# Kernel tuning notes

Hardware: AMD Instinct MI355X
Metric: run time of the kernel (lower is better)

Reference implementation:

```python
import math
import jax, jax.numpy as jnp
import numpy as np

NUM_HEADS = 16
BASE = 10000.0


def _rope_sin_cos(seq_len, head_dim):
    # theta_j = pos / base^(2j/dim), j in [0, dim//2)
    j = jnp.arange(head_dim // 2, dtype=jnp.float32)
    inv_freq = jnp.power(jnp.float32(BASE), -2.0 * j / head_dim)  # [d/2]
    pos = jnp.arange(seq_len, dtype=jnp.float32)
    ang = pos[:, None] * inv_freq[None, :]          # [S, d/2]
    sin, cos = jnp.sin(ang), jnp.cos(ang)
    # interleave-repeat each entry twice: [S, d]
    sin2 = jnp.stack([sin, sin], axis=-1).reshape(seq_len, head_dim)
    cos2 = jnp.stack([cos, cos], axis=-1).reshape(seq_len, head_dim)
    return sin2, cos2


def _apply_rope(x, sin2, cos2):
    # x: [B, H, S, d]; rotate-half interleaved: (-x1, x0, -x3, x2, ...)
    x_even, x_odd = x[..., 0::2], x[..., 1::2]
    rot = jnp.stack([-x_odd, x_even], axis=-1).reshape(x.shape)
    return x * cos2 + rot * sin2


def setup_inputs() -> dict:
    key = jax.random.key(0)
    ks = jax.random.split(key, 9)
    B, S, H = 2, 2048, 2048
    sc = 1.0 / math.sqrt(H)
    return {
        "hidden_state": jax.random.normal(ks[0], (B, S, H), jnp.float32),
        "Wq": jax.random.normal(ks[1], (H, H), jnp.float32) * sc,
        "bq": jax.random.normal(ks[2], (H,), jnp.float32) * 0.01,
        "Wk": jax.random.normal(ks[3], (H, H), jnp.float32) * sc,
        "bk": jax.random.normal(ks[4], (H,), jnp.float32) * 0.01,
        "Wv": jax.random.normal(ks[5], (H, H), jnp.float32) * sc,
        "bv": jax.random.normal(ks[6], (H,), jnp.float32) * 0.01,
        "Wo": jax.random.normal(ks[7], (H, H), jnp.float32) * sc,
        "bo": jax.random.normal(ks[8], (H,), jnp.float32) * 0.01,
    }


def reference(hidden_state, Wq, bq, Wk, bk, Wv, bv, Wo, bo):
    B, S, H = hidden_state.shape
    nh = NUM_HEADS
    hd = H // nh

    def proj(W, b):
        y = jnp.einsum('bsh,hd->bsd', hidden_state, W) + b
        return y.reshape(B, S, nh, hd).transpose(0, 2, 1, 3)  # [B,nh,S,hd]

    q = proj(Wq, bq)
    k = proj(Wk, bk)
    v = proj(Wv, bv)

    sin2, cos2 = _rope_sin_cos(S, hd)  # [S, hd]
    q = _apply_rope(q, sin2, cos2)
    k = _apply_rope(k, sin2, cos2)

    scale = 1.0 / math.sqrt(hd)
    attn = jnp.einsum('bhqd,bhkd->bhqk', q, k) * scale  # [B,nh,S,S]
    attn = jax.nn.softmax(attn, axis=-1)
    out = jnp.einsum('bhqk,bhkd->bhqd', attn, v)
    out = out.transpose(0, 2, 1, 3).reshape(B, S, H)
    return jnp.einsum('bsh,hd->bsd', out, Wo) + bo
```

## Files before the change

### kernel.cpp

```cpp
#include <hip/hip_runtime.h>
#include <math.h>


typedef __bf16 bf16;
typedef __attribute__((ext_vector_type(8))) __bf16 bf16x8;
typedef __attribute__((ext_vector_type(4))) __bf16 bf16x4;
typedef __attribute__((ext_vector_type(4))) float f32x4;

#define S_LEN 2048
#define NHEAD 16
#define HD 128

__device__ __forceinline__ f32x4 mfma16(bf16x8 a, bf16x8 b, f32x4 c) {
    return __builtin_amdgcn_mfma_f32_16x16x32_bf16(a, b, c, 0, 0, 0);
}

__global__ __launch_bounds__(256) void transpose_cvt(const float* __restrict__ W,
                                                     bf16* __restrict__ Wt,
                                                     int Kd, int Nd) {
    __shared__ float tile[32][33];
    const int tx = threadIdx.x & 31, ty = threadIdx.x >> 5;
    const int bn = blockIdx.x * 32, bk = blockIdx.y * 32;
#pragma unroll
    for (int r = 0; r < 32; r += 8)
        tile[ty + r][tx] = W[(size_t)(bk + ty + r) * Nd + bn + tx];
    __syncthreads();
#pragma unroll
    for (int r = 0; r < 32; r += 8)
        Wt[(size_t)(bn + ty + r) * Kd + bk + tx] = (bf16)tile[tx][ty + r];
}

__global__ __launch_bounds__(256)
void prep(const float* __restrict__ Wq, const float* __restrict__ Wk,
          const float* __restrict__ Wv, const float* __restrict__ Wo,
          bf16* __restrict__ Wt3, bf16* __restrict__ WoT,
          const float* __restrict__ hs, bf16* __restrict__ Xb,
          float* __restrict__ stab, float* __restrict__ ctab) {
    const int z = blockIdx.z;
    const int id = blockIdx.y * 64 + blockIdx.x;
    const int t = threadIdx.x;
    if (z == 4) {
        const int g = id * 256 + t;
        if (g < 262144) {
            const int s = g >> 7, d = g & 127;
            const float invf = exp2f(-0.20762050593046013f * (float)(d >> 1));
            float sn, cs;
            sincosf((float)s * invf, &sn, &cs);
            stab[g] = sn;
            ctab[g] = cs;
        }
        return;
    }
    if (z == 5) {
        const size_t i = ((size_t)id * 256 + t) * 8;
        const float4 v0 = *(const float4*)(hs + i);
        const float4 v1 = *(const float4*)(hs + i + 4);
        bf16x8 o;
        o[0] = (bf16)v0.x; o[1] = (bf16)v0.y; o[2] = (bf16)v0.z; o[3] = (bf16)v0.w;
        o[4] = (bf16)v1.x; o[5] = (bf16)v1.y; o[6] = (bf16)v1.z; o[7] = (bf16)v1.w;
        *(bf16x8*)(Xb + i) = o;
        return;
    }
    __shared__ float tile[32][33];
    const float* W = (z == 0) ? Wq : (z == 1) ? Wk : (z == 2) ? Wv : Wo;
    bf16* Wt = (z < 3) ? (Wt3 + (size_t)z * 2048 * 2048) : WoT;
    const int tx = t & 31, ty = t >> 5;
    const int bn = blockIdx.x * 32, bk = blockIdx.y * 32;
#pragma unroll
    for (int r = 0; r < 32; r += 8)
        tile[ty + r][tx] = W[(size_t)(bk + ty + r) * 2048 + bn + tx];
    __syncthreads();
#pragma unroll
    for (int r = 0; r < 32; r += 8)
        Wt[(size_t)(bn + ty + r) * 2048 + bk + tx] = (bf16)tile[tx][ty + r];
}

__global__ __launch_bounds__(256, 3)
void gemm_qkv(const bf16* __restrict__ A, const bf16* __restrict__ Bt,
              const float* __restrict__ bq, const float* __restrict__ bk,
              const float* __restrict__ bv, bf16* __restrict__ Qo,
              bf16* __restrict__ Ko, bf16* __restrict__ Vo,
              const float* __restrict__ stab, const float* __restrict__ ctab) {
    const int K = 2048;
    __shared__ __align__(16) bf16 smem[17408];
    bf16* As = smem;
    bf16* Bs = smem + 8192;
    const int t = threadIdx.x;
    const int w = t >> 6, l = t & 63;
    const int lr = l & 15, lq = l >> 4;
    const int m0 = blockIdx.y * 128, n0 = blockIdx.x * 128;
    const int wm = (w >> 1) * 64, wn = (w & 1) * 64;
    const int seg = n0 >> 11;
    const float* bias = (seg == 0) ? bq : (seg == 1) ? bk : bv;
    bf16* outB = (seg == 0) ? Qo : (seg == 1) ? Ko : Vo;

    f32x4 acc[4][4];
    const f32x4 fz = {0.f, 0.f, 0.f, 0.f};
#pragma unroll
    for (int i = 0; i < 4; ++i)
#pragma unroll
        for (int j = 0; j < 4; ++j) acc[i][j] = fz;

    bf16x8 rA[4], rB[4];
#pragma unroll
    for (int c = 0; c < 4; ++c) {
        const int chunk = c * 256 + t;
        const int row = chunk >> 3, cc = chunk & 7;
        rA[c] = *(const bf16x8*)&A[(size_t)(m0 + row) * K + cc * 8];
        rB[c] = *(const bf16x8*)&Bt[(size_t)(n0 + row) * K + cc * 8];
    }

    for (int k0 = 0; k0 < K; k0 += 64) {
#pragma unroll
        for (int c = 0; c < 4; ++c) {
            const int chunk = c * 256 + t;
            const int row = chunk >> 3, cc = chunk & 7;
            const int d = (row * 8 + (cc ^ (row & 7))) * 8;
            *(bf16x8*)&As[d] = rA[c];
            *(bf16x8*)&Bs[d] = rB[c];
        }
        __syncthreads();
        if (k0 + 64 < K) {
#pragma unroll
            for (int c = 0; c < 4; ++c) {
                const int chunk = c * 256 + t;
                const int row = chunk >> 3, cc = chunk & 7;
                rA[c] = *(const bf16x8*)&A[(size_t)(m0 + row) * K + k0 + 64 + cc * 8];
                rB[c] = *(const bf16x8*)&Bt[(size_t)(n0 + row) * K + k0 + 64 + cc * 8];
            }
        }
#pragma unroll
        for (int s = 0; s < 2; ++s) {
            bf16x8 af[4], bfr[4];
#pragma unroll
            for (int i = 0; i < 4; ++i) {
                const int row = wm + i * 16 + lr;
                af[i] = *(const bf16x8*)&As[(row * 8 + ((s * 4 + lq) ^ (row & 7))) * 8];
            }
#pragma unroll
            for (int j = 0; j < 4; ++j) {
                const int row = wn + j * 16 + lr;
                bfr[j] = *(const bf16x8*)&Bs[(row * 8 + ((s * 4 + lq) ^ (row & 7))) * 8];
            }
#pragma unroll
            for (int i = 0; i < 4; ++i)
#pragma unroll
                for (int j = 0; j < 4; ++j)
                    acc[i][j] = mfma16(af[i], bfr[j], acc[i][j]);
        }
        __syncthreads();
    }

    if (seg == 2) {
#pragma unroll
        for (int i = 0; i < 4; ++i) {
            const int rl0 = wm + i * 16 + lq * 4;
#pragma unroll
            for (int j = 0; j < 4; ++j) {
                const int cl = wn + j * 16 + lr;
                const float bv_ = bias[(n0 & 2047) + cl];
#pragma unroll
                for (int r = 0; r < 4; ++r)
                    smem[cl * 136 + rl0 + r] = (bf16)(acc[i][j][r] + bv_);
            }
        }
        __syncthreads();
        const int b = m0 >> 11;
#pragma unroll
        for (int p = 0; p < 8; ++p) {
            const int idx = p * 256 + t;
            const int col = idx >> 4, ch = idx & 15;
            const bf16x8 v = *(const bf16x8*)&smem[col * 136 + ch * 8];
            const int cg2 = (n0 & 2047) + col;
            const int h = cg2 >> 7, d = cg2 & 127;
            *(bf16x8*)&outB[((size_t)((b << 4) | h) * HD + d) * S_LEN +
                            (m0 & 2047) + ch * 8] = v;
        }
    } else {
#pragma unroll
        for (int i = 0; i < 4; ++i) {
            const int rg0 = m0 + wm + i * 16 + lq * 4;
#pragma unroll
            for (int j = 0; j < 4; ++j) {
                const int cg2 = (n0 & 2047) + wn + j * 16 + lr;
                const float bv_ = bias[cg2];
                const int h = cg2 >> 7, d = cg2 & 127;
#pragma unroll
                for (int r = 0; r < 4; ++r) {
                    const int rg = rg0 + r;
                    const int b = rg >> 11, s = rg & 2047;
                    float v = acc[i][j][r] + bv_;
                    float p = __shfl_xor(v, 1);
                    const float sn = stab[(s << 7) | d];
                    const float cs = ctab[(s << 7) | d];
                    float o = (d & 1) ? (v * cs + p * sn) : (v * cs - p * sn);
                    if (seg == 0) o *= 0.08838834764831843f;
                    outB[((size_t)((b << 4) + h) * S_LEN + s) * HD + d] = (bf16)o;
                }
            }
        }
    }
}

__global__ __launch_bounds__(256, 3)
void gemm_out(const bf16* __restrict__ A, const bf16* __restrict__ Bt,
              const float* __restrict__ bias, float* __restrict__ outF,
              int M, int N, int K) {
    __shared__ __align__(16) bf16 As[128 * 64];
    __shared__ __align__(16) bf16 Bs[128 * 64];
    const int t = threadIdx.x;
    const int w = t >> 6, l = t & 63;
    const int lr = l & 15, lq = l >> 4;
    const int m0 = blockIdx.y * 128, n0 = blockIdx.x * 128;
    const int wm = (w >> 1) * 64, wn = (w & 1) * 64;

    f32x4 acc[4][4];
    const f32x4 fz = {0.f, 0.f, 0.f, 0.f};
#pragma unroll
    for (int i = 0; i < 4; ++i)
#pragma unroll
        for (int j = 0; j < 4; ++j) acc[i][j] = fz;

    bf16x8 rA[4], rB[4];
#pragma unroll
    for (int c = 0; c < 4; ++c) {
        const int chunk = c * 256 + t;
        const int row = chunk >> 3, cc = chunk & 7;
        rA[c] = *(const bf16x8*)&A[(size_t)(m0 + row) * K + cc * 8];
        rB[c] = *(const bf16x8*)&Bt[(size_t)(n0 + row) * K + cc * 8];
    }

    for (int k0 = 0; k0 < K; k0 += 64) {
#pragma unroll
        for (int c = 0; c < 4; ++c) {
            const int chunk = c * 256 + t;
            const int row = chunk >> 3, cc = chunk & 7;
            const int d = (row * 8 + (cc ^ (row & 7))) * 8;
            *(bf16x8*)&As[d] = rA[c];
            *(bf16x8*)&Bs[d] = rB[c];
        }
        __syncthreads();
        if (k0 + 64 < K) {
#pragma unroll
            for (int c = 0; c < 4; ++c) {
                const int chunk = c * 256 + t;
                const int row = chunk >> 3, cc = chunk & 7;
                rA[c] = *(const bf16x8*)&A[(size_t)(m0 + row) * K + k0 + 64 + cc * 8];
                rB[c] = *(const bf16x8*)&Bt[(size_t)(n0 + row) * K + k0 + 64 + cc * 8];
            }
        }
#pragma unroll
        for (int s = 0; s < 2; ++s) {
            bf16x8 af[4], bfr[4];
#pragma unroll
            for (int i = 0; i < 4; ++i) {
                const int row = wm + i * 16 + lr;
                af[i] = *(const bf16x8*)&As[(row * 8 + ((s * 4 + lq) ^ (row & 7))) * 8];
            }
#pragma unroll
            for (int j = 0; j < 4; ++j) {
                const int row = wn + j * 16 + lr;
                bfr[j] = *(const bf16x8*)&Bs[(row * 8 + ((s * 4 + lq) ^ (row & 7))) * 8];
            }
#pragma unroll
            for (int i = 0; i < 4; ++i)
#pragma unroll
                for (int j = 0; j < 4; ++j)
                    acc[i][j] = mfma16(af[i], bfr[j], acc[i][j]);
        }
        __syncthreads();
    }
#pragma unroll
    for (int i = 0; i < 4; ++i) {
        const int rg0 = m0 + wm + i * 16 + lq * 4;
#pragma unroll
        for (int j = 0; j < 4; ++j) {
            const int cg = n0 + wn + j * 16 + lr;
            const float bv = bias[cg];
#pragma unroll
            for (int r = 0; r < 4; ++r)
                outF[(size_t)(rg0 + r) * N + cg] = acc[i][j][r] + bv;
        }
    }
}

__global__ __launch_bounds__(256, 2)
void attn_fwd(const bf16* __restrict__ Q, const bf16* __restrict__ K,
              const bf16* __restrict__ Vt, bf16* __restrict__ AO) {
    __shared__ __align__(16) bf16 Ks[64 * 128];
    __shared__ __align__(16) bf16 Vs[128 * 64];
    __shared__ __align__(16) bf16 Ps[128 * 64];
    const int t = threadIdx.x;
    const int w = t >> 6, l = t & 63;
    const int lr = l & 15, lq = l >> 4;
    const int blk = blockIdx.x;
    const int qt = (blk >> 3) & 15;
    const int bh = ((blk & 7) << 2) | (blk >> 7);
    const int b = bh >> 4, h = bh & 15;

    const bf16* Qp = Q + (size_t)bh * S_LEN * HD;
    const bf16* Kp = K + (size_t)bh * S_LEN * HD;
    const bf16* Vp = Vt + (size_t)bh * HD * S_LEN;

    bf16x8 qf[2][4];
#pragma unroll
    for (int i = 0; i < 2; ++i)
#pragma unroll
        for (int s = 0; s < 4; ++s)
            qf[i][s] = *(const bf16x8*)&Qp[(size_t)(qt * 128 + w * 32 + i * 16 + lr) * HD +
                                           s * 32 + lq * 8];

    f32x4 O[2][8];
    const f32x4 fz = {0.f, 0.f, 0.f, 0.f};
#pragma unroll
    for (int i = 0; i < 2; ++i)
#pragma unroll
        for (int jd = 0; jd < 8; ++jd) O[i][jd] = fz;
    float lst[2][4] = {{0.f, 0.f, 0.f, 0.f}, {0.f, 0.f, 0.f, 0.f}};

    bf16x8 rK[4], rV[4];
#pragma unroll
    for (int c = 0; c < 4; ++c) {
        const int chunk = c * 256 + t;
        const int kr = chunk >> 4, kc = chunk & 15;
        const int vr = chunk >> 3, vc = chunk & 7;
        rK[c] = *(const bf16x8*)&Kp[(size_t)kr * HD + kc * 8];
        rV[c] = *(const bf16x8*)&Vp[(size_t)vr * S_LEN + vc * 8];
    }

    for (int kt = 0; kt < 32; ++kt) {
#pragma unroll
        for (int c = 0; c < 4; ++c) {
            const int chunk = c * 256 + t;
            const int kr = chunk >> 4, kc = chunk & 15;
            const int vr = chunk >> 3, vc = chunk & 7;
            *(bf16x8*)&Ks[(kr * 16 + (kc ^ (kr & 15))) * 8] = rK[c];
            *(bf16x8*)&Vs[(vr * 8 + (vc ^ (vr & 7))) * 8] = rV[c];
        }
        __syncthreads();

        if (kt < 31) {
#pragma unroll
            for (int c = 0; c < 4; ++c) {
                const int chunk = c * 256 + t;
                const int kr = chunk >> 4, kc = chunk & 15;
                const int vr = chunk >> 3, vc = chunk & 7;
                rK[c] = *(const bf16x8*)&Kp[(size_t)((kt + 1) * 64 + kr) * HD + kc * 8];
                rV[c] = *(const bf16x8*)&Vp[(size_t)vr * S_LEN + (kt + 1) * 64 + vc * 8];
            }
        }

        f32x4 Sc[2][4];
#pragma unroll
        for (int i = 0; i < 2; ++i)
#pragma unroll
            for (int j = 0; j < 4; ++j) Sc[i][j] = fz;
#pragma unroll
        for (int s = 0; s < 4; ++s) {
            bf16x8 kf[4];
#pragma unroll
            for (int j = 0; j < 4; ++j) {
                const int krow = j * 16 + lr;
                kf[j] = *(const bf16x8*)&Ks[(krow * 16 + ((s * 4 + lq) ^ (krow & 15))) * 8];
            }
            __builtin_amdgcn_s_setprio(1);
#pragma unroll
            for (int i = 0; i < 2; ++i)
#pragma unroll
                for (int j = 0; j < 4; ++j)
                    Sc[i][j] = mfma16(qf[i][s], kf[j], Sc[i][j]);
            __builtin_amdgcn_s_setprio(0);
        }

#pragma unroll
        for (int i = 0; i < 2; ++i)
#pragma unroll
            for (int j = 0; j < 4; ++j)
#pragma unroll
                for (int r = 0; r < 4; ++r) {
                    const float p = __expf(Sc[i][j][r]);
                    lst[i][r] += p;
                    const int prow = w * 32 + i * 16 + lq * 4 + r;
                    const int pch = (j * 2 + (lr >> 3)) ^ (prow & 7);
                    Ps[(prow * 8 + pch) * 8 + (lr & 7)] = (bf16)p;
                }

#pragma unroll
        for (int s = 0; s < 2; ++s) {
            bf16x8 pf[2], vf[8];
#pragma unroll
            for (int i = 0; i < 2; ++i) {
                const int prow = w * 32 + i * 16 + lr;
                pf[i] = *(const bf16x8*)&Ps[(prow * 8 + ((s * 4 + lq) ^ (prow & 7))) * 8];
            }
#pragma unroll
            for (int jd = 0; jd < 8; ++jd) {
                const int vrow = jd * 16 + lr;
                vf[jd] = *(const bf16x8*)&Vs[(vrow * 8 + ((s * 4 + lq) ^ (vrow & 7))) * 8];
            }
            __builtin_amdgcn_s_setprio(1);
#pragma unroll
            for (int i = 0; i < 2; ++i)
#pragma unroll
                for (int jd = 0; jd < 8; ++jd)
                    O[i][jd] = mfma16(pf[i], vf[jd], O[i][jd]);
            __builtin_amdgcn_s_setprio(0);
        }
        __syncthreads();
    }

#pragma unroll
    for (int mask = 1; mask < 16; mask <<= 1)
#pragma unroll
        for (int i = 0; i < 2; ++i)
#pragma unroll
            for (int r = 0; r < 4; ++r) lst[i][r] += __shfl_xor(lst[i][r], mask);

#pragma unroll
    for (int i = 0; i < 2; ++i)
#pragma unroll
        for (int jd = 0; jd < 8; ++jd)
#pragma unroll
            for (int r = 0; r < 4; ++r) {
                const int srow = qt * 128 + w * 32 + i * 16 + lq * 4 + r;
                const float v = O[i][jd][r] / lst[i][r];
                AO[(size_t)(b * S_LEN + srow) * 2048 + h * HD + jd * 16 + lr] = (bf16)v;
            }
}

extern "C" void kernel_launch(void* const* d_in, const int* in_sizes, int n_in,
                              void* d_out, int out_size, void* d_ws, size_t ws_size,
                              hipStream_t stream) {
    const float* hs = (const float*)d_in[0];
    const float* Wq = (const float*)d_in[1];
    const float* bq = (const float*)d_in[2];
    const float* Wk = (const float*)d_in[3];
    const float* bk = (const float*)d_in[4];
    const float* Wv = (const float*)d_in[5];
    const float* bv = (const float*)d_in[6];
    const float* Wo = (const float*)d_in[7];
    const float* bo = (const float*)d_in[8];
    float* out = (float*)d_out;

    char* ws = (char*)d_ws;
    bf16* Xb = (bf16*)ws;
    bf16* Wt3 = (bf16*)(ws + (size_t)16777216);
    bf16* Qb = (bf16*)(ws + (size_t)41943040);
    bf16* Kb = (bf16*)(ws + (size_t)58720256);
    bf16* Vb = (bf16*)(ws + (size_t)75497472);
    float* stab = (float*)(ws + (size_t)92274688);
    float* ctab = (float*)(ws + (size_t)93323264);
    bf16* AO = Xb;

    const bool bigws = ws_size >= (size_t)102760448;
    bf16* WoT = bigws ? (bf16*)(ws + (size_t)94371840) : Wt3;

    if (bigws) {
        prep<<<dim3(64, 64, 6), 256, 0, stream>>>(Wq, Wk, Wv, Wo, Wt3, WoT,
                                                  hs, Xb, stab, ctab);
    } else {
        prep<<<dim3(64, 64, 5), 256, 0, stream>>>(Wq, Wk, Wv, Wq, Wt3, WoT,
                                                  hs, Xb, stab, ctab);
    }
    gemm_qkv<<<dim3(48, 32), 256, 0, stream>>>(Xb, Wt3, bq, bk, bv, Qb, Kb, Vb,
                                               stab, ctab);
    attn_fwd<<<512, 256, 0, stream>>>(Qb, Kb, Vb, AO);
    if (!bigws)
        transpose_cvt<<<dim3(64, 64), 256, 0, stream>>>(Wo, Wt3, 2048, 2048);
    gemm_out<<<dim3(16, 32), 256, 0, stream>>>(AO, WoT, bo, out, 4096, 2048, 2048);
}
```

Measured before the change: 392.6 us.

## Use 8 waves per attention block with 16 query rows per wave

The attention kernel moves from 4 waves handling 32 query rows each to 8 waves handling 16 rows each, with the block size doubled to 512 threads and launch bounds raised to (512,4). Per-thread registers for the Q fragments, O accumulators and score tiles are halved, and K/V staging loads are split across more threads. The aim is higher occupancy and better latency hiding. In exchange, each K/V tile loaded into LDS is reused by fewer MFMAs per wave, and the extra waves add more V fragment LDS reads and more barrier participants.

```diff
diff --git a/kernel.cpp b/kernel.cpp
--- a/kernel.cpp
+++ b/kernel.cpp
@@ -284,7 +284,7 @@
     }
 }
 
-__global__ __launch_bounds__(256, 2)
+__global__ __launch_bounds__(512, 4)
 void attn_fwd(const bf16* __restrict__ Q, const bf16* __restrict__ K,
               const bf16* __restrict__ Vt, bf16* __restrict__ AO) {
     __shared__ __align__(16) bf16 Ks[64 * 128];
@@ -302,26 +302,22 @@
     const bf16* Kp = K + (size_t)bh * S_LEN * HD;
     const bf16* Vp = Vt + (size_t)bh * HD * S_LEN;
 
-    bf16x8 qf[2][4];
-#pragma unroll
-    for (int i = 0; i < 2; ++i)
-#pragma unroll
-        for (int s = 0; s < 4; ++s)
-            qf[i][s] = *(const bf16x8*)&Qp[(size_t)(qt * 128 + w * 32 + i * 16 + lr) * HD +
-                                           s * 32 + lq * 8];
-
-    f32x4 O[2][8];
+    bf16x8 qf[4];
+#pragma unroll
+    for (int s = 0; s < 4; ++s)
+        qf[s] = *(const bf16x8*)&Qp[(size_t)(qt * 128 + w * 16 + lr) * HD +
+                                    s * 32 + lq * 8];
+
+    f32x4 O[8];
     const f32x4 fz = {0.f, 0.f, 0.f, 0.f};
 #pragma unroll
-    for (int i = 0; i < 2; ++i)
-#pragma unroll
-        for (int jd = 0; jd < 8; ++jd) O[i][jd] = fz;
-    float lst[2][4] = {{0.f, 0.f, 0.f, 0.f}, {0.f, 0.f, 0.f, 0.f}};
-
-    bf16x8 rK[4], rV[4];
-#pragma unroll
-    for (int c = 0; c < 4; ++c) {
-        const int chunk = c * 256 + t;
+    for (int jd = 0; jd < 8; ++jd) O[jd] = fz;
+    float lst[4] = {0.f, 0.f, 0.f, 0.f};
+
+    bf16x8 rK[2], rV[2];
+#pragma unroll
+    for (int c = 0; c < 2; ++c) {
+        const int chunk = c * 512 + t;
         const int kr = chunk >> 4, kc = chunk & 15;
         const int vr = chunk >> 3, vc = chunk & 7;
         rK[c] = *(const bf16x8*)&Kp[(size_t)kr * HD + kc * 8];
@@ -330,8 +326,8 @@
 
     for (int kt = 0; kt < 32; ++kt) {
 #pragma unroll
-        for (int c = 0; c < 4; ++c) {
-            const int chunk = c * 256 + t;
+        for (int c = 0; c < 2; ++c) {
+            const int chunk = c * 512 + t;
             const int kr = chunk >> 4, kc = chunk & 15;
             const int vr = chunk >> 3, vc = chunk & 7;
             *(bf16x8*)&Ks[(kr * 16 + (kc ^ (kr & 15))) * 8] = rK[c];
@@ -341,8 +337,8 @@
 
         if (kt < 31) {
 #pragma unroll
-            for (int c = 0; c < 4; ++c) {
-                const int chunk = c * 256 + t;
+            for (int c = 0; c < 2; ++c) {
+                const int chunk = c * 512 + t;
                 const int kr = chunk >> 4, kc = chunk & 15;
                 const int vr = chunk >> 3, vc = chunk & 7;
                 rK[c] = *(const bf16x8*)&Kp[(size_t)((kt + 1) * 64 + kr) * HD + kc * 8];
@@ -350,11 +346,9 @@
             }
         }
 
-        f32x4 Sc[2][4];
-#pragma unroll
-        for (int i = 0; i < 2; ++i)
-#pragma unroll
-            for (int j = 0; j < 4; ++j) Sc[i][j] = fz;
+        f32x4 Sc[4];
+#pragma unroll
+        for (int j = 0; j < 4; ++j) Sc[j] = fz;
 #pragma unroll
         for (int s = 0; s < 4; ++s) {
             bf16x8 kf[4];
@@ -365,46 +359,41 @@
             }
             __builtin_amdgcn_s_setprio(1);
 #pragma unroll
-            for (int i = 0; i < 2; ++i)
-#pragma unroll
-                for (int j = 0; j < 4; ++j)
-                    Sc[i][j] = mfma16(qf[i][s], kf[j], Sc[i][j]);
+            for (int j = 0; j < 4; ++j)
+                Sc[j] = mfma16(qf[s], kf[j], Sc[j]);
             __builtin_amdgcn_s_setprio(0);
         }
 
 #pragma unroll
-        for (int i = 0; i < 2; ++i)
-#pragma unroll
-            for (int j = 0; j < 4; ++j)
-#pragma unroll
-                for (int r = 0; r < 4; ++r) {
-                    const float p = __expf(Sc[i][j][r]);
-                    lst[i][r] += p;
-                    const int prow = w * 32 + i * 16 + lq * 4 + r;
-                    const int pch = (j * 2 + (lr >> 3)) ^ (prow & 7);
-                    Ps[(prow * 8 + pch) * 8 + (lr & 7)] = (bf16)p;
+        for (int j = 0; j < 4; ++j)
+#pragma unroll
+            for (int r = 0; r < 4; ++r) {
+                const float p = __expf(Sc[j][r]);
+                lst[r] += p;
+                const int prow = w * 16 + lq * 4 + r;
+                const int pch = (j * 2 + (lr >> 3)) ^ (prow & 7);
+                Ps[(prow * 8 + pch) * 8 + (lr & 7)] = (bf16)p;
+            }
+
+#pragma unroll
+        for (int s = 0; s < 2; ++s) {
+            const int prow = w * 16 + lr;
+            const bf16x8 pf =
+                *(const bf16x8*)&Ps[(prow * 8 + ((s * 4 + lq) ^ (prow & 7))) * 8];
+#pragma unroll
+            for (int jh = 0; jh < 2; ++jh) {
+                bf16x8 vf[4];
+#pragma unroll
+                for (int jj = 0; jj < 4; ++jj) {
+                    const int vrow = (jh * 4 + jj) * 16 + lr;
+                    vf[jj] = *(const bf16x8*)&Vs[(vrow * 8 + ((s * 4 + lq) ^ (vrow & 7))) * 8];
                 }
-
-#pragma unroll
-        for (int s = 0; s < 2; ++s) {
-            bf16x8 pf[2], vf[8];
-#pragma unroll
-            for (int i = 0; i < 2; ++i) {
-                const int prow = w * 32 + i * 16 + lr;
-                pf[i] = *(const bf16x8*)&Ps[(prow * 8 + ((s * 4 + lq) ^ (prow & 7))) * 8];
-            }
-#pragma unroll
-            for (int jd = 0; jd < 8; ++jd) {
-                const int vrow = jd * 16 + lr;
-                vf[jd] = *(const bf16x8*)&Vs[(vrow * 8 + ((s * 4 + lq) ^ (vrow & 7))) * 8];
-            }
-            __builtin_amdgcn_s_setprio(1);
-#pragma unroll
-            for (int i = 0; i < 2; ++i)
-#pragma unroll
-                for (int jd = 0; jd < 8; ++jd)
-                    O[i][jd] = mfma16(pf[i], vf[jd], O[i][jd]);
-            __builtin_amdgcn_s_setprio(0);
+                __builtin_amdgcn_s_setprio(1);
+#pragma unroll
+                for (int jj = 0; jj < 4; ++jj)
+                    O[jh * 4 + jj] = mfma16(pf, vf[jj], O[jh * 4 + jj]);
+                __builtin_amdgcn_s_setprio(0);
+            }
         }
         __syncthreads();
     }
@@ -412,20 +401,16 @@
 #pragma unroll
     for (int mask = 1; mask < 16; mask <<= 1)
 #pragma unroll
-        for (int i = 0; i < 2; ++i)
-#pragma unroll
-            for (int r = 0; r < 4; ++r) lst[i][r] += __shfl_xor(lst[i][r], mask);
-
-#pragma unroll
-    for (int i = 0; i < 2; ++i)
-#pragma unroll
-        for (int jd = 0; jd < 8; ++jd)
-#pragma unroll
-            for (int r = 0; r < 4; ++r) {
-                const int srow = qt * 128 + w * 32 + i * 16 + lq * 4 + r;
-                const float v = O[i][jd][r] / lst[i][r];
-                AO[(size_t)(b * S_LEN + srow) * 2048 + h * HD + jd * 16 + lr] = (bf16)v;
-            }
+        for (int r = 0; r < 4; ++r) lst[r] += __shfl_xor(lst[r], mask);
+
+#pragma unroll
+    for (int jd = 0; jd < 8; ++jd)
+#pragma unroll
+        for (int r = 0; r < 4; ++r) {
+            const int srow = qt * 128 + w * 16 + lq * 4 + r;
+            const float v = O[jd][r] / lst[r];
+            AO[(size_t)(b * S_LEN + srow) * 2048 + h * HD + jd * 16 + lr] = (bf16)v;
+        }
 }
 
 extern "C" void kernel_launch(void* const* d_in, const int* in_sizes, int n_in,
@@ -464,7 +449,7 @@
     }
     gemm_qkv<<<dim3(48, 32), 256, 0, stream>>>(Xb, Wt3, bq, bk, bv, Qb, Kb, Vb,
                                                stab, ctab);
-    attn_fwd<<<512, 256, 0, stream>>>(Qb, Kb, Vb, AO);
+    attn_fwd<<<512, 512, 0, stream>>>(Qb, Kb, Vb, AO);
     if (!bigws)
         transpose_cvt<<<dim3(64, 64), 256, 0, stream>>>(Wo, Wt3, 2048, 2048);
     gemm_out<<<dim3(16, 32), 256, 0, stream>>>(AO, WoT, bo, out, 4096, 2048, 2048);
```

After: 402.1 us. +2.4%, slower.
